# Performance work log

Hardware: AMD Instinct MI355X
Metric: run time of the kernel (lower is better)

Reference implementation:

```python
import jax, jax.numpy as jnp
import numpy as np
from jax import lax

C = 128; H = 28; W = 28
VID_LENS = [32, 96, 64, 48, 80, 40, 88, 64]  # sums to 512
T_TOTAL = sum(VID_LENS)


def setup_inputs() -> dict:
    key = jax.random.key(0)
    ks = jax.random.split(key, 6)
    fan2 = C * 9
    fan1 = C * 3
    return {
        "x": jax.random.normal(ks[0], (T_TOTAL, C, H, W), dtype=jnp.float32),
        "vid_lens": jnp.array(VID_LENS, dtype=jnp.int32),
        "w_sp": jax.random.normal(ks[1], (C, C, 3, 3), dtype=jnp.float32) / np.sqrt(fan2),
        "b_sp": jax.random.normal(ks[2], (C,), dtype=jnp.float32) * 0.01,
        "w_t": jax.random.normal(ks[3], (C, C, 3), dtype=jnp.float32) / np.sqrt(fan1),
        "b_t": jax.random.normal(ks[4], (C,), dtype=jnp.float32) * 0.01,
        "alpha": jnp.full((C,), 0.25, dtype=jnp.float32),  # MultiNL ~ per-channel PReLU
    }


def _forward(x, vid_lens, w_sp, b_sp, w_t, b_t, alpha):
    projection = x
    # spatial 3x3 conv, stride 1, padding 1 (SAME), NCHW
    y = lax.conv_general_dilated(
        x, w_sp, window_strides=(1, 1), padding="SAME",
        dimension_numbers=("NCHW", "OIHW", "NCHW")) + b_sp[None, :, None, None]

    # Ragged temporal conv1d (k=3, pad=1) over concatenated time axis.
    # Zero the temporal neighbors at segment boundaries so each video is
    # convolved independently (equivalent to per-segment zero padding).
    T = y.shape[0]
    ends = jnp.cumsum(vid_lens)            # segment end indices (exclusive)
    starts = ends - vid_lens               # segment start indices
    start_mask = jnp.zeros((T,), bool).at[starts].set(True)
    end_mask = jnp.zeros((T,), bool).at[ends - 1].set(True)

    y_prev = jnp.where(start_mask[:, None, None, None], 0.0, jnp.roll(y, 1, axis=0))
    y_next = jnp.where(end_mask[:, None, None, None], 0.0, jnp.roll(y, -1, axis=0))

    # conv1d along time == per-tap channel-mixing matmul
    z = (jnp.einsum("oc,tchw->tohw", w_t[:, :, 0], y_prev)
         + jnp.einsum("oc,tchw->tohw", w_t[:, :, 1], y)
         + jnp.einsum("oc,tchw->tohw", w_t[:, :, 2], y_next)
         + b_t[None, :, None, None])

    # MultiNL modeled as per-channel PReLU
    z = jnp.where(z >= 0, z, alpha[None, :, None, None] * z)
    return z + projection


def reference(x, vid_lens, w_sp, b_sp, w_t, b_t, alpha):
    out = _forward(x, vid_lens, w_sp, b_sp, w_t, b_t, alpha)
    return (out, vid_lens)  # lengths are unchanged (k=3, pad=1)
```

## Files before the change

kernel.cpp:

```cpp
#include <hip/hip_runtime.h>

#define TT   512
#define CH   128
#define HWP  784
#define NSEG 8
#define NOUT 51380224

typedef short bf16x8  __attribute__((ext_vector_type(8)));
typedef float f32x4   __attribute__((ext_vector_type(4)));
typedef float f32x16  __attribute__((ext_vector_type(16)));
typedef int   i32x4   __attribute__((ext_vector_type(4)));
typedef unsigned short u16x4 __attribute__((ext_vector_type(4)));
typedef unsigned short u16x8 __attribute__((ext_vector_type(8)));

__device__ inline unsigned short f2bf(float f) {
    unsigned u = __builtin_bit_cast(unsigned, f);
    u += 0x7fffu + ((u >> 16) & 1u);
    return (unsigned short)(u >> 16);
}

__device__ inline void gld_lds16(const void* g, void* l) {
    __builtin_amdgcn_global_load_lds(
        (const __attribute__((address_space(1))) void*)g,
        (__attribute__((address_space(3))) void*)l, 16, 0, 0);
}

#define MFMA32(A, B, C) __builtin_amdgcn_mfma_f32_32x32x16_bf16(A, B, C, 0, 0, 0)

__global__ void repack_wsp(const float* __restrict__ w, short* __restrict__ wA) {
    int s = blockIdx.x * 256 + threadIdx.x;
    if (s >= 128 * 128 * 9) return;
    int co = s / 1152, r = s % 1152, ci = r / 9, kh = (r % 9) / 3, kw = r % 3;
    int tap = kh * 3 + kw;
    int m = co >> 5, row = co & 31;
    int ks = ci >> 4, kgrp = (ci >> 3) & 1, e = ci & 7;
    int lane = kgrp * 32 + row;
    int dst = (((tap * 8 + ks) * 4 + m) * 64 + lane) * 8 + e;
    wA[dst] = (short)f2bf(w[s]);
}

__global__ void repack_wt2(const float* __restrict__ w, short* __restrict__ wAt) {
    int s = blockIdx.x * 256 + threadIdx.x;
    if (s >= 128 * 128 * 3) return;
    int o = s / 384, r = s % 384, i = r / 3, tap = r % 3;
    int dst = tap * 16384 + (o >> 4) * 2048 + (i >> 5) * 512 +
              ((i >> 3) & 3) * 128 + (o & 15) * 8 + (i & 7);
    wAt[dst] = (short)f2bf(w[s]);
}

__global__ __launch_bounds__(256, 3) void spatial_mfma(
    const float* __restrict__ x, const short* __restrict__ wA,
    const float* __restrict__ b_sp, unsigned short* __restrict__ yT)
{
    __shared__ __align__(16) short xs[7 * 30 * 128];
    char* xsb = (char*)xs;
    const int t = blockIdx.y;
    const int rg = blockIdx.x >> 1, hf = blockIdx.x & 1;
    const int r0 = rg * 8;
    const int rows = (28 - r0 < 8) ? (28 - r0) : 8;
    const int pxcnt = rows * 28;
    if (hf * 128 >= pxcnt) return;
    const int tid = threadIdx.x;
    const int wstart = r0 + hf * 4 - 1;

    for (int u = tid; u < 4032; u += 256) {
        if (u < 3136) {
            int cp = u & 63, q = u >> 6;
            int rl = q / 7, g = q % 7;
            int rr = wstart + rl;
            float4 f0 = make_float4(0.f, 0.f, 0.f, 0.f), f1 = f0;
            if (rr >= 0 && rr < 28) {
                const float* px0 = &x[((size_t)(t * CH + 2 * cp)) * HWP + rr * 28 + g * 4];
                f0 = *(const float4*)px0;
                f1 = *(const float4*)(px0 + HWP);
            }
            float a0[4] = {f0.x, f0.y, f0.z, f0.w}, a1[4] = {f1.x, f1.y, f1.z, f1.w};
            int stb = rl * 30 + g * 4 + 1;
#pragma unroll
            for (int j = 0; j < 4; ++j) {
                int st = stb + j;
                unsigned val = (unsigned)f2bf(a0[j]) | ((unsigned)f2bf(a1[j]) << 16);
                int addr = (st << 8) | (((cp >> 2) ^ (st & 15)) << 4) | ((cp & 3) << 2);
                *(unsigned*)(xsb + addr) = val;
            }
        } else {
            int v = u - 3136;
            int cp = v & 63, k = v >> 6;
            int st = (k >> 1) * 30 + (k & 1) * 29;
            int addr = (st << 8) | (((cp >> 2) ^ (st & 15)) << 4) | ((cp & 3) << 2);
            *(unsigned*)(xsb + addr) = 0u;
        }
    }
    __syncthreads();

    const int wid = tid >> 6, l = tid & 63;
    const int l31 = l & 31, bb5 = l >> 5;
    const int ch = wid & 1, pg = wid >> 1;
    const int ch2 = ch * 2;
    const int tI0 = hf * 4 + pg * 2, tI1 = tI0 + 1;
    const int p0 = tI0 * 32 + l31, p1 = tI1 * 32 + l31;
    const int pc0 = (p0 < pxcnt) ? p0 : hf * 128;
    const int pc1 = (p1 < pxcnt) ? p1 : hf * 128;
    const int st0_0 = (pc0 / 28 - hf * 4 + 1) * 30 + pc0 % 28 + 1;
    const int st0_1 = (pc1 / 28 - hf * 4 + 1) * 30 + pc1 % 28 + 1;

    f32x16 zz = {};
    f32x16 acc00 = zz, acc10 = zz, acc01 = zz, acc11 = zz;

    const bf16x8* wv = (const bf16x8*)wA;

    auto ldB = [&](int it, int s0) -> i32x4 {
        int tap = it >> 3;
        int off = (tap / 3 - 1) * 30 + (tap % 3) - 1;
        int stv = s0 + off;
        int addr = (stv << 8) | ((((it & 7) * 2 + bb5) ^ (stv & 15)) << 4);
        return *(const i32x4*)(xsb + addr);
    };

    i32x4 B0a = ldB(0, st0_0), B0b = ldB(0, st0_1);
    i32x4 B1a = ldB(1, st0_0), B1b = ldB(1, st0_1);
    bf16x8 A0a = wv[(0 * 4 + ch2) * 64 + l], A0b = wv[(0 * 4 + ch2 + 1) * 64 + l];
    bf16x8 A1a = wv[(1 * 4 + ch2) * 64 + l], A1b = wv[(1 * 4 + ch2 + 1) * 64 + l];

#pragma unroll
    for (int it = 0; it < 72; ++it) {
        int nx = (it + 2 < 72) ? (it + 2) : 70;
        i32x4 nBa = ldB(nx, st0_0), nBb = ldB(nx, st0_1);
        bf16x8 nAa = wv[(nx * 4 + ch2) * 64 + l];
        bf16x8 nAb = wv[(nx * 4 + ch2 + 1) * 64 + l];

        bf16x8 fa = __builtin_bit_cast(bf16x8, B0a);
        bf16x8 fb = __builtin_bit_cast(bf16x8, B0b);
        __builtin_amdgcn_s_setprio(1);
        acc00 = MFMA32(A0a, fa, acc00);
        acc10 = MFMA32(A0b, fa, acc10);
        acc01 = MFMA32(A0a, fb, acc01);
        acc11 = MFMA32(A0b, fb, acc11);
        __builtin_amdgcn_s_setprio(0);

        B0a = B1a; B0b = B1b; B1a = nBa; B1b = nBb;
        A0a = A1a; A0b = A1b; A1a = nAa; A1b = nAb;
    }

    __syncthreads();
    const int wbase = wid * 8704;
#pragma unroll
    for (int mi = 0; mi < 2; ++mi) {
        f32x16 aT0 = mi ? acc10 : acc00;
        f32x16 aT1 = mi ? acc11 : acc01;
#pragma unroll
        for (int r2 = 0; r2 < 4; ++r2) {
            int cb = (ch2 + mi) * 32 + 8 * r2 + 4 * bb5;
            float4 bs = *(const float4*)&b_sp[cb];
            float bsa[4] = {bs.x, bs.y, bs.z, bs.w};
            u16x4 k0, k1;
#pragma unroll
            for (int q = 0; q < 4; ++q) {
                k0[q] = f2bf(aT0[r2 * 4 + q] + bsa[q]);
                k1[q] = f2bf(aT1[r2 * 4 + q] + bsa[q]);
            }
            int co_off = (mi * 32 + 8 * r2 + 4 * bb5) * 2;
            *(u16x4*)(xsb + wbase + l31 * 136 + co_off) = k0;
            *(u16x4*)(xsb + wbase + 4352 + l31 * 136 + co_off) = k1;
        }
    }
#pragma unroll
    for (int tt2 = 0; tt2 < 2; ++tt2) {
        int tI = tt2 ? tI1 : tI0;
#pragma unroll
        for (int j = 0; j < 4; ++j) {
            int idx = j * 64 + l;
            int px = idx >> 3, sub = idx & 7;
            u16x8 v = *(const u16x8*)(xsb + wbase + tt2 * 4352 + px * 136 + sub * 16);
            int p = tI * 32 + px;
            if (p < pxcnt) {
                char* dst = (char*)yT + ((size_t)t * HWP + r0 * 28 + p) * 256 +
                            ch * 128 + sub * 16;
                *(u16x8*)dst = v;
            }
        }
    }
}

__global__ __launch_bounds__(256, 4) void temporal_mfma(
    const unsigned short* __restrict__ yT, const short* __restrict__ wAt,
    const float* __restrict__ b_t, const float* __restrict__ alpha,
    const float* __restrict__ x, const int* __restrict__ vid_lens,
    float* __restrict__ out)
{
    __shared__ __align__(16) char ldsT[29696];

    const int chunk = blockIdx.x, t = blockIdx.y;
    const int tid = threadIdx.x, wid = tid >> 6, l = tid & 63;
    const int l15 = l & 15, kgrp = l >> 4;
    const int sx = l15 & 7;

    bool isS = false, isE = false;
    {
        int cum = 0;
        for (int s = 0; s < NSEG; ++s) {
            if (t == cum) isS = true;
            cum += vid_lens[s];
            if (t == cum - 1) isE = true;
        }
    }
    const bool tapAct[3] = {!isS, true, !isE};

    auto stage = [&](int s) {
        int tap = s >> 1, kp = s & 1;
        if (!tapAct[tap]) return;
        int tp = t + tap - 1;
        const char* yb = (const char*)yT + (size_t)tp * HWP * 256;
        char* buf = ldsT + (s & 1) * 14336;
#pragma unroll
        for (int r = 0; r < 4; ++r) {
            int c = r * 256 + wid * 64 + l;
            if (r < 3 || wid < 2) {
                int px = c >> 3, sp = c & 7;
                int ssrc = sp ^ (px & 7);
                const char* g = yb + ((size_t)(chunk * 112 + px)) * 256 + kp * 128 + ssrc * 16;
                char* ldst = buf + (r * 256 + wid * 64) * 16;
                gld_lds16(g, ldst);
            }
        }
    };

    f32x4 acc[2][7];
#pragma unroll
    for (int m = 0; m < 2; ++m)
#pragma unroll
        for (int n = 0; n < 7; ++n) acc[m][n] = (f32x4){0.f, 0.f, 0.f, 0.f};

    const bf16x8* wAv = (const bf16x8*)wAt;

    stage(0);
    __syncthreads();

    for (int s = 0; s < 6; ++s) {
        if (s < 5) stage(s + 1);
        int tap = s >> 1, kp = s & 1;
        if (tapAct[tap]) {
            const char* buf = ldsT + (s & 1) * 14336;
            bf16x8 a[2][2];
#pragma unroll
            for (int m = 0; m < 2; ++m)
#pragma unroll
                for (int k1 = 0; k1 < 2; ++k1)
                    a[m][k1] = wAv[((tap * 8 + wid * 2 + m) * 4 + kp * 2 + k1) * 64 + l];
            __builtin_amdgcn_s_setprio(1);
#pragma unroll
            for (int k1 = 0; k1 < 2; ++k1) {
#pragma unroll
                for (int nf = 0; nf < 7; ++nf) {
                    int addr = (nf * 16 + l15) * 128 + ((k1 * 4 + kgrp) ^ sx) * 16;
                    i32x4 bi = *(const i32x4*)(buf + addr);
                    bf16x8 b = __builtin_bit_cast(bf16x8, bi);
                    acc[0][nf] = __builtin_amdgcn_mfma_f32_16x16x32_bf16(a[0][k1], b, acc[0][nf], 0, 0, 0);
                    acc[1][nf] = __builtin_amdgcn_mfma_f32_16x16x32_bf16(a[1][k1], b, acc[1][nf], 0, 0, 0);
                }
            }
            __builtin_amdgcn_s_setprio(0);
        }
        __syncthreads();
    }

    float* fl = (float*)ldsT;
    const int wbase = wid * 1856;
#pragma unroll
    for (int m = 0; m < 2; ++m) {
#pragma unroll
        for (int nf = 0; nf < 7; ++nf)
#pragma unroll
            for (int rr = 0; rr < 4; ++rr)
                fl[wbase + (kgrp * 4 + rr) * 116 + nf * 16 + l15] = acc[m][nf][rr];
#pragma unroll
        for (int j = 0; j < 7; ++j) {
            int idx = j * 64 + l;
            int co_r = idx / 28, q = idx % 28;
            f32x4 v4 = *(const f32x4*)&fl[wbase + co_r * 116 + q * 4];
            int co_g = wid * 32 + m * 16 + co_r;
            float bt = b_t[co_g], al = alpha[co_g];
            size_t gi = ((size_t)(t * CH + co_g)) * HWP + chunk * 112 + q * 4;
            float4 xv = *(const float4*)&x[gi];
            float xr[4] = {xv.x, xv.y, xv.z, xv.w};
            float rrv[4];
#pragma unroll
            for (int e = 0; e < 4; ++e) {
                float v = v4[e] + bt;
                v = (v >= 0.f) ? v : al * v;
                rrv[e] = v + xr[e];
            }
            *(float4*)&out[gi] = make_float4(rrv[0], rrv[1], rrv[2], rrv[3]);
        }
        __syncthreads();
    }
}

__global__ void write_lens(const int* __restrict__ vid_lens, float* __restrict__ out) {
    int i = threadIdx.x;
    if (i < NSEG) out[NOUT + i] = (float)vid_lens[i];
}

extern "C" void kernel_launch(void* const* d_in, const int* in_sizes, int n_in,
                              void* d_out, int out_size, void* d_ws, size_t ws_size,
                              hipStream_t stream) {
    const float* x        = (const float*)d_in[0];
    const int*   vid_lens = (const int*)d_in[1];
    const float* w_sp     = (const float*)d_in[2];
    const float* b_sp     = (const float*)d_in[3];
    const float* w_t      = (const float*)d_in[4];
    const float* b_t      = (const float*)d_in[5];
    const float* alpha    = (const float*)d_in[6];
    float* out = (float*)d_out;

    unsigned short* yT = (unsigned short*)d_ws;
    short* wA  = (short*)((char*)d_ws + 102760448);
    short* wAt = (short*)((char*)d_ws + 102760448 + 294912);

    repack_wsp<<<576, 256, 0, stream>>>(w_sp, wA);
    repack_wt2<<<192, 256, 0, stream>>>(w_t, wAt);
    spatial_mfma<<<dim3(8, 512), 256, 0, stream>>>(x, wA, b_sp, yT);
    temporal_mfma<<<dim3(7, 512), 256, 0, stream>>>(yT, wAt, b_t, alpha, x, vid_lens, out);
    write_lens<<<1, 64, 0, stream>>>(vid_lens, out);
}
```

Baseline: 341.4 us.

## Enlarge spatial conv tile to 8 rows per block with 2x4 MFMA register tile

The spatial 3x3 conv block now covers a full 8-row group (up to 224 pixels) instead of half of it, so each block stages 10 halo rows instead of 6. The per-warp output tile grows from 2x2 to 2x4 MFMA tiles, and the weight fragments are loaded once per tap for all four pixel tiles. This cuts halo reload overhead and raises the ratio of MFMAs to weight and LDS loads. In exchange the kernel uses more LDS and registers, occupancy drops from 3 to 2 blocks, and it loses the explicit two-stage software prefetch.

```diff
diff --git a/kernel.cpp b/kernel.cpp
--- a/kernel.cpp
+++ b/kernel.cpp
@@ -48,48 +48,43 @@
     wAt[dst] = (short)f2bf(w[s]);
 }
 
-__global__ __launch_bounds__(256, 3) void spatial_mfma(
+__global__ __launch_bounds__(256, 2) void spatial_mfma(
     const float* __restrict__ x, const short* __restrict__ wA,
     const float* __restrict__ b_sp, unsigned short* __restrict__ yT)
 {
-    __shared__ __align__(16) short xs[7 * 30 * 128];
+    __shared__ __align__(16) short xs[300 * 128];
     char* xsb = (char*)xs;
     const int t = blockIdx.y;
-    const int rg = blockIdx.x >> 1, hf = blockIdx.x & 1;
-    const int r0 = rg * 8;
+    const int r0 = blockIdx.x * 8;
     const int rows = (28 - r0 < 8) ? (28 - r0) : 8;
     const int pxcnt = rows * 28;
-    if (hf * 128 >= pxcnt) return;
     const int tid = threadIdx.x;
-    const int wstart = r0 + hf * 4 - 1;
-
-    for (int u = tid; u < 4032; u += 256) {
-        if (u < 3136) {
-            int cp = u & 63, q = u >> 6;
-            int rl = q / 7, g = q % 7;
-            int rr = wstart + rl;
-            float4 f0 = make_float4(0.f, 0.f, 0.f, 0.f), f1 = f0;
-            if (rr >= 0 && rr < 28) {
-                const float* px0 = &x[((size_t)(t * CH + 2 * cp)) * HWP + rr * 28 + g * 4];
-                f0 = *(const float4*)px0;
-                f1 = *(const float4*)(px0 + HWP);
-            }
-            float a0[4] = {f0.x, f0.y, f0.z, f0.w}, a1[4] = {f1.x, f1.y, f1.z, f1.w};
-            int stb = rl * 30 + g * 4 + 1;
-#pragma unroll
-            for (int j = 0; j < 4; ++j) {
-                int st = stb + j;
-                unsigned val = (unsigned)f2bf(a0[j]) | ((unsigned)f2bf(a1[j]) << 16);
-                int addr = (st << 8) | (((cp >> 2) ^ (st & 15)) << 4) | ((cp & 3) << 2);
-                *(unsigned*)(xsb + addr) = val;
-            }
-        } else {
-            int v = u - 3136;
-            int cp = v & 63, k = v >> 6;
-            int st = (k >> 1) * 30 + (k & 1) * 29;
+
+    for (int u = tid; u < 4480; u += 256) {
+        int cp = u & 63, q = u >> 6;
+        int rl = q / 7, g = q % 7;
+        int rr = r0 - 1 + rl;
+        float4 f0 = make_float4(0.f, 0.f, 0.f, 0.f), f1 = f0;
+        if (rr >= 0 && rr < 28) {
+            const float* px0 = &x[((size_t)(t * CH + 2 * cp)) * HWP + rr * 28 + g * 4];
+            f0 = *(const float4*)px0;
+            f1 = *(const float4*)(px0 + HWP);
+        }
+        float a0[4] = {f0.x, f0.y, f0.z, f0.w}, a1[4] = {f1.x, f1.y, f1.z, f1.w};
+        int stb = rl * 30 + g * 4 + 1;
+#pragma unroll
+        for (int j = 0; j < 4; ++j) {
+            int st = stb + j;
+            unsigned val = (unsigned)f2bf(a0[j]) | ((unsigned)f2bf(a1[j]) << 16);
             int addr = (st << 8) | (((cp >> 2) ^ (st & 15)) << 4) | ((cp & 3) << 2);
-            *(unsigned*)(xsb + addr) = 0u;
-        }
+            *(unsigned*)(xsb + addr) = val;
+        }
+    }
+    for (int v = tid; v < 1280; v += 256) {
+        int cp = v & 63, k = v >> 6;
+        int st = (k >> 1) * 30 + (k & 1) * 29;
+        int addr = (st << 8) | (((cp >> 2) ^ (st & 15)) << 4) | ((cp & 3) << 2);
+        *(unsigned*)(xsb + addr) = 0u;
     }
     __syncthreads();
 
@@ -97,82 +92,84 @@
     const int l31 = l & 31, bb5 = l >> 5;
     const int ch = wid & 1, pg = wid >> 1;
     const int ch2 = ch * 2;
-    const int tI0 = hf * 4 + pg * 2, tI1 = tI0 + 1;
-    const int p0 = tI0 * 32 + l31, p1 = tI1 * 32 + l31;
-    const int pc0 = (p0 < pxcnt) ? p0 : hf * 128;
-    const int pc1 = (p1 < pxcnt) ? p1 : hf * 128;
-    const int st0_0 = (pc0 / 28 - hf * 4 + 1) * 30 + pc0 % 28 + 1;
-    const int st0_1 = (pc1 / 28 - hf * 4 + 1) * 30 + pc1 % 28 + 1;
+
+    int st0[4];
+#pragma unroll
+    for (int ti = 0; ti < 4; ++ti) {
+        int p = (pg * 4 + ti) * 32 + l31;
+        int pc = (p < pxcnt) ? p : 0;
+        st0[ti] = (pc / 28 + 1) * 30 + pc % 28 + 1;
+    }
 
     f32x16 zz = {};
-    f32x16 acc00 = zz, acc10 = zz, acc01 = zz, acc11 = zz;
+    f32x16 acc[2][4];
+#pragma unroll
+    for (int mi = 0; mi < 2; ++mi)
+#pragma unroll
+        for (int ti = 0; ti < 4; ++ti) acc[mi][ti] = zz;
 
     const bf16x8* wv = (const bf16x8*)wA;
 
-    auto ldB = [&](int it, int s0) -> i32x4 {
-        int tap = it >> 3;
-        int off = (tap / 3 - 1) * 30 + (tap % 3) - 1;
-        int stv = s0 + off;
-        int addr = (stv << 8) | ((((it & 7) * 2 + bb5) ^ (stv & 15)) << 4);
-        return *(const i32x4*)(xsb + addr);
-    };
-
-    i32x4 B0a = ldB(0, st0_0), B0b = ldB(0, st0_1);
-    i32x4 B1a = ldB(1, st0_0), B1b = ldB(1, st0_1);
-    bf16x8 A0a = wv[(0 * 4 + ch2) * 64 + l], A0b = wv[(0 * 4 + ch2 + 1) * 64 + l];
-    bf16x8 A1a = wv[(1 * 4 + ch2) * 64 + l], A1b = wv[(1 * 4 + ch2 + 1) * 64 + l];
-
-#pragma unroll
-    for (int it = 0; it < 72; ++it) {
-        int nx = (it + 2 < 72) ? (it + 2) : 70;
-        i32x4 nBa = ldB(nx, st0_0), nBb = ldB(nx, st0_1);
-        bf16x8 nAa = wv[(nx * 4 + ch2) * 64 + l];
-        bf16x8 nAb = wv[(nx * 4 + ch2 + 1) * 64 + l];
-
-        bf16x8 fa = __builtin_bit_cast(bf16x8, B0a);
-        bf16x8 fb = __builtin_bit_cast(bf16x8, B0b);
-        __builtin_amdgcn_s_setprio(1);
-        acc00 = MFMA32(A0a, fa, acc00);
-        acc10 = MFMA32(A0b, fa, acc10);
-        acc01 = MFMA32(A0a, fb, acc01);
-        acc11 = MFMA32(A0b, fb, acc11);
-        __builtin_amdgcn_s_setprio(0);
-
-        B0a = B1a; B0b = B1b; B1a = nBa; B1b = nBb;
-        A0a = A1a; A0b = A1b; A1a = nAa; A1b = nAb;
+    for (int tap = 0; tap < 9; ++tap) {
+        const int off = (tap / 3 - 1) * 30 + (tap % 3) - 1;
+        int rb[4], sw[4];
+#pragma unroll
+        for (int ti = 0; ti < 4; ++ti) {
+            int stv = st0[ti] + off;
+            rb[ti] = stv << 8;
+            sw[ti] = stv & 15;
+        }
+        bf16x8 A[16];
+#pragma unroll
+        for (int k2 = 0; k2 < 16; ++k2)
+            A[k2] = wv[((tap * 8 + (k2 >> 1)) * 4 + ch2 + (k2 & 1)) * 64 + l];
+
+#pragma unroll
+        for (int ks = 0; ks < 8; ++ks) {
+            i32x4 b[4];
+#pragma unroll
+            for (int ti = 0; ti < 4; ++ti)
+                b[ti] = *(const i32x4*)(xsb + (rb[ti] | (((2 * ks + bb5) ^ sw[ti]) << 4)));
+            __builtin_amdgcn_s_setprio(1);
+#pragma unroll
+            for (int ti = 0; ti < 4; ++ti) {
+                bf16x8 bf = __builtin_bit_cast(bf16x8, b[ti]);
+                acc[0][ti] = MFMA32(A[ks * 2], bf, acc[0][ti]);
+                acc[1][ti] = MFMA32(A[ks * 2 + 1], bf, acc[1][ti]);
+            }
+            __builtin_amdgcn_s_setprio(0);
+        }
     }
 
     __syncthreads();
-    const int wbase = wid * 8704;
-#pragma unroll
-    for (int mi = 0; mi < 2; ++mi) {
-        f32x16 aT0 = mi ? acc10 : acc00;
-        f32x16 aT1 = mi ? acc11 : acc01;
-#pragma unroll
-        for (int r2 = 0; r2 < 4; ++r2) {
-            int cb = (ch2 + mi) * 32 + 8 * r2 + 4 * bb5;
-            float4 bs = *(const float4*)&b_sp[cb];
-            float bsa[4] = {bs.x, bs.y, bs.z, bs.w};
-            u16x4 k0, k1;
-#pragma unroll
-            for (int q = 0; q < 4; ++q) {
-                k0[q] = f2bf(aT0[r2 * 4 + q] + bsa[q]);
-                k1[q] = f2bf(aT1[r2 * 4 + q] + bsa[q]);
-            }
-            int co_off = (mi * 32 + 8 * r2 + 4 * bb5) * 2;
-            *(u16x4*)(xsb + wbase + l31 * 136 + co_off) = k0;
-            *(u16x4*)(xsb + wbase + 4352 + l31 * 136 + co_off) = k1;
-        }
-    }
-#pragma unroll
-    for (int tt2 = 0; tt2 < 2; ++tt2) {
-        int tI = tt2 ? tI1 : tI0;
+    const int wbase = wid * 17408;
+#pragma unroll
+    for (int ti = 0; ti < 4; ++ti) {
+#pragma unroll
+        for (int mi = 0; mi < 2; ++mi) {
+#pragma unroll
+            for (int r2 = 0; r2 < 4; ++r2) {
+                int cb = (ch2 + mi) * 32 + 8 * r2 + 4 * bb5;
+                float4 bs = *(const float4*)&b_sp[cb];
+                float bsa[4] = {bs.x, bs.y, bs.z, bs.w};
+                u16x4 k;
+#pragma unroll
+                for (int q = 0; q < 4; ++q)
+                    k[q] = f2bf(acc[mi][ti][r2 * 4 + q] + bsa[q]);
+                int co_off = (mi * 32 + 8 * r2 + 4 * bb5) * 2;
+                *(u16x4*)(xsb + wbase + ti * 4352 + l31 * 136 + co_off) = k;
+            }
+        }
+    }
+#pragma unroll
+    for (int ti = 0; ti < 4; ++ti) {
+        int tI = pg * 4 + ti;
 #pragma unroll
         for (int j = 0; j < 4; ++j) {
             int idx = j * 64 + l;
-            int px = idx >> 3, sub = idx & 7;
-            u16x8 v = *(const u16x8*)(xsb + wbase + tt2 * 4352 + px * 136 + sub * 16);
-            int p = tI * 32 + px;
+            int pxl = idx >> 3, sub = idx & 7;
+            u16x8 v = *(const u16x8*)(xsb + wbase + ti * 4352 + pxl * 136 + sub * 16);
+            int p = tI * 32 + pxl;
             if (p < pxcnt) {
                 char* dst = (char*)yT + ((size_t)t * HWP + r0 * 28 + p) * 256 +
                             ch * 128 + sub * 16;
@@ -319,7 +316,7 @@
 
     repack_wsp<<<576, 256, 0, stream>>>(w_sp, wA);
     repack_wt2<<<192, 256, 0, stream>>>(w_t, wAt);
-    spatial_mfma<<<dim3(8, 512), 256, 0, stream>>>(x, wA, b_sp, yT);
+    spatial_mfma<<<dim3(4, 512), 256, 0, stream>>>(x, wA, b_sp, yT);
     temporal_mfma<<<dim3(7, 512), 256, 0, stream>>>(yT, wAt, b_t, alpha, x, vid_lens, out);
     write_lens<<<1, 64, 0, stream>>>(vid_lens, out);
 }
```

New measurement: 336.6 us. No clear change (-1.4%).
